# Performance work log

Measured on AMD Instinct MI355X. Metric: run time of the kernel, lower is better.

Reference implementation:

```python
import jax, jax.numpy as jnp
import numpy as np

S, B, N, A, L = 2, 8, 12, 4, 24
C, AUX, EK, K, M, OTH = 256, 16, 64, 256, 8, 32
D2 = C + AUX          # transfromer2 d_model
FF = 2048             # torch TransformerEncoderLayer default dim_feedforward
RIN = 2 * EK + 2 * D2 + 2 * OTH
NLAYERS = 2


def _layernorm(x, g, b, eps=1e-5):
    mu = x.mean(-1, keepdims=True)
    var = ((x - mu) ** 2).mean(-1, keepdims=True)
    return (x - mu) * jax.lax.rsqrt(var + eps) * g + b


def _mha(x, Wq, bq, Wk, bk, Wv, bv, Wo, bo):
    # x: [seq, batch, d]; single head (nhead=1), torch seq-first semantics
    q = x @ Wq.T + bq
    k = x @ Wk.T + bk
    v = x @ Wv.T + bv
    scale = x.shape[-1] ** -0.5
    att = jax.nn.softmax(jnp.einsum('sbd,tbd->bst', q, k) * scale, axis=-1)
    o = jnp.einsum('bst,tbd->sbd', att, v)
    return o @ Wo.T + bo


def _encoder(x, aw, ab, w1, b1, w2, b2, lg, lb):
    # post-norm torch TransformerEncoderLayer, ReLU FFN, dropout off (eval)
    for i in range(aw.shape[0]):
        a = _mha(x, aw[i, 0], ab[i, 0], aw[i, 1], ab[i, 1], aw[i, 2], ab[i, 2], aw[i, 3], ab[i, 3])
        x = _layernorm(x + a, lg[i, 0], lb[i, 0])
        h = jax.nn.relu(x @ w1[i].T + b1[i]) @ w2[i].T + b2[i]
        x = _layernorm(x + h, lg[i, 1], lb[i, 1])
    return x


def _conv(x, w, b, pad):
    y = jax.lax.conv_general_dilated(x, w, (1, 1), [(pad, pad), (0, 0)],
                                     dimension_numbers=('NCHW', 'OIHW', 'NCHW'))
    return y + b[None, :, None, None]


def _forward(chars, att_type, kw_idx, input_idx, static, other,
             char_table, filter_w, filter_b, gate_w, gate_b, mlp_w, mlp_b,
             kw_table, aline_w, aline_b,
             t1_attn_w, t1_attn_b, t1_ffn_w1, t1_ffn_b1, t1_ffn_w2, t1_ffn_b2, t1_ln_g, t1_ln_b,
             t2_attn_w, t2_attn_b, t2_ffn_w1, t2_ffn_b1, t2_ffn_w2, t2_ffn_b2, t2_ln_g, t2_ln_b,
             reg_w1, reg_b1, reg_w2, reg_b2):
    # nn.Embedding(max_norm=1): rows renormalized to norm <= 1
    nrm = jnp.linalg.norm(char_table, axis=1, keepdims=True)
    tbl = char_table * jnp.minimum(1.0, 1.0 / jnp.maximum(nrm, 1e-7))
    ce = tbl[chars]                                  # [S,B,N,A,L,C]
    x = ce.reshape(-1, 1, L, C)                      # strings as conv batch
    f = jnp.tanh(_conv(x, filter_w, filter_b, 1))    # gated conv: tanh * sigmoid
    g = jax.nn.sigmoid(_conv(x, gate_w, gate_b, 1))
    v = _conv(f * g, mlp_w, mlp_b, 0)                # 1x1 conv back to 1 channel
    str_vec = v.reshape(S, B, N, A, L, C).mean(axis=4)   # mean over chars -> [S,B,N,A,C]
    kw_vec = kw_table[kw_idx] @ aline_w.T + aline_b      # keyword path -> [S,B,N,A,C]
    att_vec = jnp.where((att_type == 1)[..., None], kw_vec, str_vec)
    # transfromer1: torch seq-first, seq = nodes, batch = (side, plan, attr)
    x1 = att_vec.transpose(2, 0, 1, 3, 4).reshape(N, S * B * A, C)
    y1 = _encoder(x1, t1_attn_w, t1_attn_b, t1_ffn_w1, t1_ffn_b1, t1_ffn_w2, t1_ffn_b2, t1_ln_g, t1_ln_b)
    node_enc = y1.reshape(N, S, B, A, C).mean(axis=3).transpose(1, 2, 0, 3)  # mean over attrs -> [S,B,N,C]
    h = jnp.concatenate([node_enc, static], axis=-1)                          # [S,B,N,D2]
    # transfromer2: seq = plan batch, batch = (side, node) -- torch seq-first
    x2 = h.transpose(1, 0, 2, 3).reshape(B, S * N, D2)
    y2 = _encoder(x2, t2_attn_w, t2_attn_b, t2_ffn_w1, t2_ffn_b1, t2_ffn_w2, t2_ffn_b2, t2_ln_g, t2_ln_b)
    real = y2.reshape(B, S, N, D2).mean(axis=2)      # mean over nodes -> [B,S,D2]
    inp = kw_table[input_idx].mean(axis=2)           # encoding_input -> [S,B,EK]
    feats = jnp.concatenate([inp[0], real[:, 0], inp[1], real[:, 1], other], axis=1)  # [B,RIN]
    return jax.nn.relu(feats @ reg_w1.T + reg_b1) @ reg_w2.T + reg_b2  # [B,1]


def setup_inputs() -> dict:
    key = jax.random.key(0)
    ks = iter(jax.random.split(key, 64))
    def rn(shape, s=0.02):
        return jax.random.normal(next(ks), shape, jnp.float32) * s
    inp = {
        'chars': jax.random.randint(next(ks), (S, B, N, A, L), 0, 128, jnp.int32),
        'att_type': jax.random.randint(next(ks), (S, B, N, A), 0, 2, jnp.int32),
        'kw_idx': jax.random.randint(next(ks), (S, B, N, A), 0, K, jnp.int32),
        'input_idx': jax.random.randint(next(ks), (S, B, M), 0, K, jnp.int32),
        'static': rn((S, B, N, AUX), 1.0),
        'other': rn((B, 2 * OTH), 1.0),
        'char_table': rn((128, C), 1.0),
        'filter_w': rn((16, 1, 3, 1), 0.2), 'filter_b': rn((16,), 0.02),
        'gate_w': rn((16, 1, 3, 1), 0.2), 'gate_b': rn((16,), 0.02),
        'mlp_w': rn((1, 16, 1, 1), 0.2), 'mlp_b': rn((1,), 0.02),
        'kw_table': rn((K, EK), 0.05),
        'aline_w': rn((C, EK), 0.05), 'aline_b': rn((C,), 0.02),
        't1_attn_w': rn((NLAYERS, 4, C, C), 0.05), 't1_attn_b': rn((NLAYERS, 4, C), 0.02),
        't1_ffn_w1': rn((NLAYERS, FF, C), 0.02), 't1_ffn_b1': rn((NLAYERS, FF), 0.02),
        't1_ffn_w2': rn((NLAYERS, C, FF), 0.02), 't1_ffn_b2': rn((NLAYERS, C), 0.02),
        't1_ln_g': jnp.ones((NLAYERS, 2, C), jnp.float32), 't1_ln_b': jnp.zeros((NLAYERS, 2, C), jnp.float32),
        't2_attn_w': rn((NLAYERS, 4, D2, D2), 0.05), 't2_attn_b': rn((NLAYERS, 4, D2), 0.02),
        't2_ffn_w1': rn((NLAYERS, FF, D2), 0.02), 't2_ffn_b1': rn((NLAYERS, FF), 0.02),
        't2_ffn_w2': rn((NLAYERS, D2, FF), 0.02), 't2_ffn_b2': rn((NLAYERS, D2), 0.02),
        't2_ln_g': jnp.ones((NLAYERS, 2, D2), jnp.float32), 't2_ln_b': jnp.zeros((NLAYERS, 2, D2), jnp.float32),
        'reg_w1': rn((32, RIN), 0.05), 'reg_b1': rn((32,), 0.02),
        'reg_w2': rn((1, 32), 0.1), 'reg_b2': rn((1,), 0.02),
    }
    return inp


def reference(chars, att_type, kw_idx, input_idx, static, other,
              char_table, filter_w, filter_b, gate_w, gate_b, mlp_w, mlp_b,
              kw_table, aline_w, aline_b,
              t1_attn_w, t1_attn_b, t1_ffn_w1, t1_ffn_b1, t1_ffn_w2, t1_ffn_b2, t1_ln_g, t1_ln_b,
              t2_attn_w, t2_attn_b, t2_ffn_w1, t2_ffn_b1, t2_ffn_w2, t2_ffn_b2, t2_ln_g, t2_ln_b,
              reg_w1, reg_b1, reg_w2, reg_b2):
    return _forward(chars, att_type, kw_idx, input_idx, static, other,
                    char_table, filter_w, filter_b, gate_w, gate_b, mlp_w, mlp_b,
                    kw_table, aline_w, aline_b,
                    t1_attn_w, t1_attn_b, t1_ffn_w1, t1_ffn_b1, t1_ffn_w2, t1_ffn_b2, t1_ln_g, t1_ln_b,
                    t2_attn_w, t2_attn_b, t2_ffn_w1, t2_ffn_b1, t2_ffn_w2, t2_ffn_b2, t2_ln_g, t2_ln_b,
                    reg_w1, reg_b1, reg_w2, reg_b2)
```

## Files before the change

kernel.cpp:

```cpp
#include <hip/hip_runtime.h>
#include <math.h>

#define S_ 2
#define B_ 8
#define N_ 12
#define A_ 4
#define L_ 24
#define C_ 256
#define AUX_ 16
#define EK_ 64
#define K_ 256
#define M_ 8
#define OTH_ 32
#define D2_ 272
#define FF_ 2048
#define RIN_ 736
#define NSTR_ (S_*B_*N_*A_)

typedef __attribute__((ext_vector_type(8))) short short8v;
typedef __attribute__((ext_vector_type(4))) float f32x4;

__device__ __forceinline__ unsigned short f2bf(float f) {
    unsigned u = __float_as_uint(f);
    return (unsigned short)((u + 0x7FFFu + ((u >> 16) & 1u)) >> 16);
}

__global__ void cvt_w_k(const float* __restrict__ s0, const float* __restrict__ s1,
                        const float* __restrict__ s2, const float* __restrict__ s3,
                        const float* __restrict__ s4, const float* __restrict__ s5,
                        unsigned short* __restrict__ dst) {
    const int T = 5441536 / 4;
    for (int q = blockIdx.x * 256 + threadIdx.x; q < T; q += gridDim.x * 256) {
        int idx = q * 4;
        const float* src; int off;
        if      (idx < 524288)  { src = s0; off = 0; }
        else if (idx < 1572864) { src = s1; off = 524288; }
        else if (idx < 2621440) { src = s2; off = 1572864; }
        else if (idx < 3213312) { src = s3; off = 2621440; }
        else if (idx < 4327424) { src = s4; off = 3213312; }
        else                    { src = s5; off = 4327424; }
        float4 v = *(const float4*)(src + (idx - off));
        ushort4 o;
        o.x = f2bf(v.x); o.y = f2bf(v.y); o.z = f2bf(v.z); o.w = f2bf(v.w);
        *(ushort4*)(dst + idx) = o;
    }
}

__global__ void scale_table_k(const float* __restrict__ tbl, float* __restrict__ out) {
    int r = blockIdx.x;
    int c = threadIdx.x;
    float v = tbl[r * C_ + c];
    float sq = v * v;
    for (int off = 32; off; off >>= 1) sq += __shfl_down(sq, off);
    __shared__ float red[4];
    __shared__ float scl;
    if ((c & 63) == 0) red[c >> 6] = sq;
    __syncthreads();
    if (c == 0) {
        float n = sqrtf(red[0] + red[1] + red[2] + red[3]);
        scl = fminf(1.f, 1.f / fmaxf(n, 1e-7f));
    }
    __syncthreads();
    out[r * C_ + c] = v * scl;
}

__global__ void attvec_k(const int* __restrict__ chars, const int* __restrict__ att_type,
                         const int* __restrict__ kw_idx, const float* __restrict__ tblS,
                         const float* __restrict__ fw, const float* __restrict__ fb,
                         const float* __restrict__ gw, const float* __restrict__ gb,
                         const float* __restrict__ mw, const float* __restrict__ mb,
                         const float* __restrict__ kwt, const float* __restrict__ aw,
                         const float* __restrict__ ab, float* __restrict__ x1,
                         unsigned short* __restrict__ x1b, int* __restrict__ ctr) {
    int tid = threadIdx.x;
    int grp = tid >> 8;
    int c = tid & 255;
    __shared__ int su;
    __shared__ int ch[L_];
    __shared__ float xv[L_ + 2][C_];
    __shared__ float part[4][C_];

    const float L2E = 1.44269504f;
    float f0[4], f1[4], f2[4], fbv[4], g0[4], g1[4], g2[4], gbv[4], mwv[4];
    #pragma unroll
    for (int oo = 0; oo < 4; ++oo) {
        int o = grp * 4 + oo;
        f0[oo] = 2.f*L2E*fw[o*3]; f1[oo] = 2.f*L2E*fw[o*3+1]; f2[oo] = 2.f*L2E*fw[o*3+2];
        fbv[oo] = 2.f*L2E*fb[o];
        g0[oo] = L2E*gw[o*3]; g1[oo] = L2E*gw[o*3+1]; g2[oo] = L2E*gw[o*3+2];
        gbv[oo] = L2E*gb[o];
        mwv[oo] = mw[o];
    }

    for (;;) {
        if (tid == 0) su = atomicAdd(ctr, 1);
        __syncthreads();
        int str = su;
        if (str >= NSTR_) break;
        bool kw = (att_type[str] == 1);
        float partial;
        if (kw) {
            const float* kr = kwt + kw_idx[str] * EK_ + grp * 16;
            const float* awr = aw + c * EK_ + grp * 16;
            float acc = (grp == 0) ? ab[c] : 0.f;
            #pragma unroll
            for (int e = 0; e < 16; ++e) acc = fmaf(kr[e], awr[e], acc);
            partial = acc;
        } else {
            if (tid < L_) ch[tid] = chars[str * L_ + tid];
            __syncthreads();
            #pragma unroll
            for (int i = 0; i < 6; ++i) {
                int l = grp * 6 + i;
                xv[l + 1][c] = tblS[ch[l] * C_ + c];
            }
            if (grp == 0) xv[0][c] = 0.f;
            if (grp == 3) xv[L_ + 1][c] = 0.f;
            __syncthreads();

            float osum[4] = {0.f, 0.f, 0.f, 0.f};
            float xm = xv[0][c], x0 = xv[1][c];
            for (int l = 1; l <= L_; ++l) {
                float xp = xv[l + 1][c];
                #pragma unroll
                for (int oo = 0; oo < 4; ++oo) {
                    float pf2 = fbv[oo] + f0[oo]*xm + f1[oo]*x0 + f2[oo]*xp;
                    float pg  = gbv[oo] + g0[oo]*xm + g1[oo]*x0 + g2[oo]*xp;
                    pf2 = fminf(fmaxf(pf2, -43.f), 43.f);
                    pg  = fminf(fmaxf(pg,  -22.f), 22.f);
                    float e1 = __builtin_amdgcn_exp2f(pf2);
                    float e2 = __builtin_amdgcn_exp2f(pg);
                    float num = (e1 - 1.f) * e2;
                    float den = (e1 + 1.f) * (e2 + 1.f);
                    osum[oo] = fmaf(num, __builtin_amdgcn_rcpf(den), osum[oo]);
                }
                xm = x0; x0 = xp;
            }
            partial = mwv[0]*osum[0] + mwv[1]*osum[1] + mwv[2]*osum[2] + mwv[3]*osum[3];
            __syncthreads();
        }
        part[grp][c] = partial;
        __syncthreads();
        if (grp == 0) {
            int a = str & 3;
            int n = (str >> 2) % N_;
            int sb = str / (N_ * A_);
            int row = n * 64 + sb * 4 + a;
            float tot = part[0][c] + part[1][c] + part[2][c] + part[3][c];
            float out = kw ? tot : (mb[0] + tot * (1.f / 24.f));
            x1[row * C_ + c] = out;
            x1b[row * C_ + c] = f2bf(out);
        }
        __syncthreads();
    }
}

__global__ void gemm_mfma_k(const unsigned short* __restrict__ Ab,
                            const unsigned short* __restrict__ Wb,
                            const float* __restrict__ bias, float* __restrict__ Cf,
                            unsigned short* __restrict__ Cb,
                            int R, int K, int N, int relu, int kslice, int obf) {
    int tid = threadIdx.x;
    int wave = tid >> 6, lane = tid & 63;
    int fr = lane & 15, fq = lane >> 4;
    int m0 = blockIdx.y * 64;
    int n0 = blockIdx.x * 64 + wave * 16;
    int kbeg = blockIdx.z * kslice;
    int kend = min(kbeg + kslice, K);
    int col = n0 + fr;
    bool bok = col < N;
    const unsigned short* Wrow = Wb + (size_t)col * K;
    const unsigned short* Ar0 = Ab + (size_t)(m0 + fr) * K;
    const unsigned short* Ar1 = Ab + (size_t)(m0 + 16 + fr) * K;
    const unsigned short* Ar2 = Ab + (size_t)(m0 + 32 + fr) * K;
    const unsigned short* Ar3 = Ab + (size_t)(m0 + 48 + fr) * K;

    f32x4 acc0 = {0.f,0.f,0.f,0.f}, acc1 = {0.f,0.f,0.f,0.f};
    f32x4 acc2 = {0.f,0.f,0.f,0.f}, acc3 = {0.f,0.f,0.f,0.f};
    const short8v z8 = {0,0,0,0,0,0,0,0};
    short8v pb, pa0, pa1, pa2, pa3;

#define LDSET(ktv) do {                                                   \
        int kl2 = (ktv) + fq * 8;                                         \
        bool kv2 = (kl2 + 8 <= kend);                                     \
        pb  = (bok && kv2) ? *(const short8v*)(Wrow + kl2) : z8;          \
        pa0 = kv2 ? *(const short8v*)(Ar0 + kl2) : z8;                    \
        pa1 = kv2 ? *(const short8v*)(Ar1 + kl2) : z8;                    \
        pa2 = kv2 ? *(const short8v*)(Ar2 + kl2) : z8;                    \
        pa3 = kv2 ? *(const short8v*)(Ar3 + kl2) : z8;                    \
    } while (0)

    LDSET(kbeg);
    for (int kt = kbeg; kt < kend; kt += 32) {
        short8v bf = pb, af0 = pa0, af1 = pa1, af2 = pa2, af3 = pa3;
        if (kt + 32 < kend) LDSET(kt + 32);
        acc0 = __builtin_amdgcn_mfma_f32_16x16x32_bf16(af0, bf, acc0, 0, 0, 0);
        acc1 = __builtin_amdgcn_mfma_f32_16x16x32_bf16(af1, bf, acc1, 0, 0, 0);
        acc2 = __builtin_amdgcn_mfma_f32_16x16x32_bf16(af2, bf, acc2, 0, 0, 0);
        acc3 = __builtin_amdgcn_mfma_f32_16x16x32_bf16(af3, bf, acc3, 0, 0, 0);
    }
#undef LDSET

    if (!bok) return;
    bool direct = (gridDim.z == 1);
    float bv = direct ? bias[col] : 0.f;
    float* outf = direct ? Cf : (Cf + (size_t)blockIdx.z * R * N);
#define STOREACC(accv, mi) do {                                           \
        _Pragma("unroll")                                                 \
        for (int j = 0; j < 4; ++j) {                                     \
            int row = m0 + (mi)*16 + fq * 4 + j;                          \
            float v = accv[j] + bv;                                       \
            if (direct && relu) v = fmaxf(v, 0.f);                        \
            if (obf) Cb[(size_t)row * N + col] = f2bf(v);                 \
            else     outf[(size_t)row * N + col] = v;                     \
        }                                                                 \
    } while (0)
    STOREACC(acc0, 0); STOREACC(acc1, 1); STOREACC(acc2, 2); STOREACC(acc3, 3);
#undef STOREACC
}

__global__ void attn_k(const float* __restrict__ qkv, unsigned short* __restrict__ ob,
                       int seq, int batch, int d, float scale) {
    __shared__ float sm[3 * 12 * 260];
    __shared__ float sc[12 * 12];
    int j = blockIdx.x, tid = threadIdx.x;
    int dp = d + 4;
    int s3 = 3 * d;
    float* qs = sm;
    float* ks = sm + 12 * 260;
    float* vs = sm + 2 * 12 * 260;
    for (int idx = tid; idx < seq * d; idx += 256) {
        int s = idx / d, cc = idx - s * d;
        const float* base = qkv + (size_t)(s * batch + j) * s3 + cc;
        qs[s * dp + cc] = base[0];
        ks[s * dp + cc] = base[d];
        vs[s * dp + cc] = base[2 * d];
    }
    __syncthreads();
    for (int p4 = tid; p4 < seq * seq * 4; p4 += 256) {
        int p = p4 >> 2, sub = p4 & 3;
        int s = p / seq, t = p - s * seq;
        const float* qp = qs + s * dp;
        const float* kp = ks + t * dp;
        float acc = 0.f;
        for (int cc = sub; cc < d; cc += 4) acc = fmaf(qp[cc], kp[cc], acc);
        acc += __shfl_xor(acc, 1);
        acc += __shfl_xor(acc, 2);
        if (sub == 0) sc[p] = acc * scale;
    }
    __syncthreads();
    if (tid < seq) {
        float m = -1e30f;
        for (int t = 0; t < seq; ++t) m = fmaxf(m, sc[tid * seq + t]);
        float ssum = 0.f;
        for (int t = 0; t < seq; ++t) {
            float e = __expf(sc[tid * seq + t] - m);
            sc[tid * seq + t] = e;
            ssum += e;
        }
        float inv = 1.f / ssum;
        for (int t = 0; t < seq; ++t) sc[tid * seq + t] *= inv;
    }
    __syncthreads();
    for (int c = tid; c < d; c += 256) {
        for (int s = 0; s < seq; ++s) {
            float acc = 0.f;
            for (int t = 0; t < seq; ++t) acc = fmaf(sc[s * seq + t], vs[t * dp + c], acc);
            ob[(size_t)(s * batch + j) * d + c] = f2bf(acc);
        }
    }
}

__global__ void redln_k(const float* __restrict__ part, const float* __restrict__ bias,
                        float* __restrict__ x, unsigned short* __restrict__ xb,
                        const float* __restrict__ g, const float* __restrict__ b,
                        int d, int NS, int RN) {
    int r = blockIdx.x, tid = threadIdx.x;
    __shared__ float red[10];
    const float* xr = x + (size_t)r * d;
    int i0 = tid, i1 = tid + 256;
    bool h0 = i0 < d, h1 = i1 < d;
    float v0 = 0.f, v1 = 0.f;
    if (h0) {
        v0 = xr[i0] + bias[i0];
        for (int z = 0; z < NS; ++z) v0 += part[(size_t)z * RN + (size_t)r * d + i0];
    }
    if (h1) {
        v1 = xr[i1] + bias[i1];
        for (int z = 0; z < NS; ++z) v1 += part[(size_t)z * RN + (size_t)r * d + i1];
    }
    float s = v0 + v1, ss = v0 * v0 + v1 * v1;
    for (int off = 32; off; off >>= 1) {
        s += __shfl_down(s, off);
        ss += __shfl_down(ss, off);
    }
    if ((tid & 63) == 0) { red[(tid >> 6) * 2] = s; red[(tid >> 6) * 2 + 1] = ss; }
    __syncthreads();
    if (tid == 0) {
        float S = red[0] + red[2] + red[4] + red[6];
        float SS = red[1] + red[3] + red[5] + red[7];
        float mu = S / d;
        float var = SS / d - mu * mu;
        red[8] = mu;
        red[9] = rsqrtf(var + 1e-5f);
    }
    __syncthreads();
    float mu = red[8], inv = red[9];
    float* xw = x + (size_t)r * d;
    if (h0) {
        float o = (v0 - mu) * inv * g[i0] + b[i0];
        xw[i0] = o; xb[(size_t)r * d + i0] = f2bf(o);
    }
    if (h1) {
        float o = (v1 - mu) * inv * g[i1] + b[i1];
        xw[i1] = o; xb[(size_t)r * d + i1] = f2bf(o);
    }
}

__global__ void build_x2_k(const float* __restrict__ y1, const float* __restrict__ stat,
                           float* __restrict__ x2, unsigned short* __restrict__ x2b) {
    int id = blockIdx.x;
    int n = id % N_;
    int b = (id / N_) % B_;
    int s = id / (N_ * B_);
    int orow = b * (S_ * N_) + s * N_ + n;
    for (int c = threadIdx.x; c < D2_; c += 256) {
        float v;
        if (c < C_) {
            int j0 = (s * B_ + b) * A_;
            float acc = 0.f;
            for (int a = 0; a < A_; ++a) acc += y1[(size_t)(n * 64 + j0 + a) * C_ + c];
            v = acc * 0.25f;
        } else {
            v = stat[((size_t)(s * B_ + b) * N_ + n) * AUX_ + (c - C_)];
        }
        x2[(size_t)orow * D2_ + c] = v;
        x2b[(size_t)orow * D2_ + c] = f2bf(v);
    }
}

__global__ void build_real_k(const float* __restrict__ y2, float* __restrict__ real) {
    int id = blockIdx.x;
    int s = id & 1, b = id >> 1;
    for (int c = threadIdx.x; c < D2_; c += 256) {
        float acc = 0.f;
        for (int n = 0; n < N_; ++n) acc += y2[(size_t)(b * 24 + s * N_ + n) * D2_ + c];
        real[(size_t)(b * 2 + s) * D2_ + c] = acc * (1.f / 12.f);
    }
}

__global__ void regressor_k(const float* __restrict__ real, const int* __restrict__ input_idx,
                            const float* __restrict__ kwt, const float* __restrict__ other,
                            const float* __restrict__ w1, const float* __restrict__ b1,
                            const float* __restrict__ w2, const float* __restrict__ b2,
                            float* __restrict__ out) {
    int b = blockIdx.x;
    int tid = threadIdx.x;
    __shared__ float feats[RIN_];
    __shared__ float hh[32];
    for (int i = tid; i < RIN_; i += 256) {
        float v;
        if (i < 64) {
            float acc = 0.f;
            for (int m = 0; m < M_; ++m) acc += kwt[input_idx[b * M_ + m] * EK_ + i];
            v = acc * 0.125f;
        } else if (i < 336) {
            v = real[(size_t)(b * 2 + 0) * D2_ + (i - 64)];
        } else if (i < 400) {
            int e = i - 336;
            float acc = 0.f;
            for (int m = 0; m < M_; ++m) acc += kwt[input_idx[64 + b * M_ + m] * EK_ + e];
            v = acc * 0.125f;
        } else if (i < 672) {
            v = real[(size_t)(b * 2 + 1) * D2_ + (i - 400)];
        } else {
            v = other[b * 64 + (i - 672)];
        }
        feats[i] = v;
    }
    __syncthreads();
    if (tid < 32) {
        float acc = b1[tid];
        const float* wr = w1 + (size_t)tid * RIN_;
        for (int i = 0; i < RIN_; ++i) acc += feats[i] * wr[i];
        hh[tid] = fmaxf(acc, 0.f);
    }
    __syncthreads();
    if (tid == 0) {
        float acc = b2[0];
        for (int j = 0; j < 32; ++j) acc += hh[j] * w2[j];
        out[b] = acc;
    }
}

extern "C" void kernel_launch(void* const* d_in, const int* in_sizes, int n_in,
                              void* d_out, int out_size, void* d_ws, size_t ws_size,
                              hipStream_t stream) {
    const int*   chars      = (const int*)d_in[0];
    const int*   att_type   = (const int*)d_in[1];
    const int*   kw_idx     = (const int*)d_in[2];
    const int*   input_idx  = (const int*)d_in[3];
    const float* stat       = (const float*)d_in[4];
    const float* other      = (const float*)d_in[5];
    const float* char_table = (const float*)d_in[6];
    const float* filter_w   = (const float*)d_in[7];
    const float* filter_b   = (const float*)d_in[8];
    const float* gate_w     = (const float*)d_in[9];
    const float* gate_b     = (const float*)d_in[10];
    const float* mlp_w      = (const float*)d_in[11];
    const float* mlp_b      = (const float*)d_in[12];
    const float* kw_table   = (const float*)d_in[13];
    const float* aline_w    = (const float*)d_in[14];
    const float* aline_b    = (const float*)d_in[15];
    const float* t1_attn_w  = (const float*)d_in[16];
    const float* t1_attn_b  = (const float*)d_in[17];
    const float* t1_ffn_w1  = (const float*)d_in[18];
    const float* t1_ffn_b1  = (const float*)d_in[19];
    const float* t1_ffn_w2  = (const float*)d_in[20];
    const float* t1_ffn_b2  = (const float*)d_in[21];
    const float* t1_ln_g    = (const float*)d_in[22];
    const float* t1_ln_b    = (const float*)d_in[23];
    const float* t2_attn_w  = (const float*)d_in[24];
    const float* t2_attn_b  = (const float*)d_in[25];
    const float* t2_ffn_w1  = (const float*)d_in[26];
    const float* t2_ffn_b1  = (const float*)d_in[27];
    const float* t2_ffn_w2  = (const float*)d_in[28];
    const float* t2_ffn_b2  = (const float*)d_in[29];
    const float* t2_ln_g    = (const float*)d_in[30];
    const float* t2_ln_b    = (const float*)d_in[31];
    const float* reg_w1     = (const float*)d_in[32];
    const float* reg_b1     = (const float*)d_in[33];
    const float* reg_w2     = (const float*)d_in[34];
    const float* reg_b2     = (const float*)d_in[35];

    float* ws   = (float*)d_ws;
    float* tblS = ws;
    float* x1   = tblS + 32768;
    float* qkv  = x1 + 196608;
    float* pbuf = qkv + 589824;
    float* x2   = pbuf + 786432;
    float* realb= x2 + 52224;
    unsigned short* x1b = (unsigned short*)(realb + 4352);
    unsigned short* obb = x1b + 196608;
    unsigned short* hb  = obb + 196608;
    unsigned short* x2b = hb + 1572864;
    unsigned short* wbf = x2b + 52224 + 16;
    unsigned short* wb_t1_attn = wbf;
    unsigned short* wb_t1_ffn1 = wbf + 524288;
    unsigned short* wb_t1_ffn2 = wbf + 1572864;
    unsigned short* wb_t2_attn = wbf + 2621440;
    unsigned short* wb_t2_ffn1 = wbf + 3213312;
    unsigned short* wb_t2_ffn2 = wbf + 4327424;
    int* ctr = (int*)(wbf + 5441536);

    auto gemm_f32 = [&](const unsigned short* A, const unsigned short* Wb, const float* bias,
                        float* Cc, int R, int Kk, int N) {
        dim3 g((N + 63) / 64, R / 64, 1);
        gemm_mfma_k<<<g, 256, 0, stream>>>(A, Wb, bias, Cc, (unsigned short*)0,
                                           R, Kk, N, 0, Kk, 0);
    };
    auto gemm_bf16 = [&](const unsigned short* A, const unsigned short* Wb, const float* bias,
                         unsigned short* Cc, int R, int Kk, int N) {
        dim3 g((N + 63) / 64, R / 64, 1);
        gemm_mfma_k<<<g, 256, 0, stream>>>(A, Wb, bias, (float*)0, Cc,
                                           R, Kk, N, 1, Kk, 1);
    };
    auto gemm_split_ln = [&](const unsigned short* A, const unsigned short* Wb,
                             const float* bias, float* x, unsigned short* xb,
                             const float* g, const float* b,
                             int R, int Kk, int N, int ns) {
        int ksl = ((Kk + ns - 1) / ns + 31) / 32 * 32;
        dim3 gr((N + 63) / 64, R / 64, ns);
        gemm_mfma_k<<<gr, 256, 0, stream>>>(A, Wb, bias, pbuf, (unsigned short*)0,
                                            R, Kk, N, 0, ksl, 0);
        redln_k<<<R, 256, 0, stream>>>(pbuf, bias, x, xb, g, b, N, ns, R * N);
    };

    hipMemsetAsync(ctr, 0, sizeof(int), stream);
    cvt_w_k<<<2048, 256, 0, stream>>>(t1_attn_w, t1_ffn_w1, t1_ffn_w2,
                                      t2_attn_w, t2_ffn_w1, t2_ffn_w2, wbf);
    scale_table_k<<<128, 256, 0, stream>>>(char_table, tblS);
    attvec_k<<<512, 1024, 0, stream>>>(chars, att_type, kw_idx, tblS,
                                       filter_w, filter_b, gate_w, gate_b,
                                       mlp_w, mlp_b, kw_table, aline_w, aline_b,
                                       x1, x1b, ctr);

    for (int i = 0; i < 2; ++i) {
        const unsigned short* awb = wb_t1_attn + (size_t)i * 4 * C_ * C_;
        const float* ab = t1_attn_b + (size_t)i * 4 * C_;
        gemm_f32(x1b, awb, ab, qkv, 768, C_, 3 * C_);
        attn_k<<<64, 256, 0, stream>>>(qkv, obb, 12, 64, C_, 0.0625f);
        gemm_split_ln(obb, awb + 3 * C_ * C_, ab + 3 * C_, x1, x1b,
                      t1_ln_g + i * 2 * C_, t1_ln_b + i * 2 * C_, 768, C_, C_, 2);
        gemm_bf16(x1b, wb_t1_ffn1 + (size_t)i * FF_ * C_, t1_ffn_b1 + i * FF_, hb, 768, C_, FF_);
        gemm_split_ln(hb, wb_t1_ffn2 + (size_t)i * C_ * FF_, t1_ffn_b2 + i * C_, x1, x1b,
                      t1_ln_g + i * 2 * C_ + C_, t1_ln_b + i * 2 * C_ + C_, 768, FF_, C_, 4);
    }

    build_x2_k<<<192, 256, 0, stream>>>(x1, stat, x2, x2b);

    float sc2 = 1.0f / sqrtf(272.0f);
    for (int i = 0; i < 2; ++i) {
        const unsigned short* awb = wb_t2_attn + (size_t)i * 4 * D2_ * D2_;
        const float* ab = t2_attn_b + (size_t)i * 4 * D2_;
        gemm_f32(x2b, awb, ab, qkv, 192, D2_, 3 * D2_);
        attn_k<<<24, 256, 0, stream>>>(qkv, obb, 8, 24, D2_, sc2);
        gemm_split_ln(obb, awb + 3 * D2_ * D2_, ab + 3 * D2_, x2, x2b,
                      t2_ln_g + i * 2 * D2_, t2_ln_b + i * 2 * D2_, 192, D2_, D2_, 4);
        gemm_bf16(x2b, wb_t2_ffn1 + (size_t)i * FF_ * D2_, t2_ffn_b1 + i * FF_, hb, 192, D2_, FF_);
        gemm_split_ln(hb, wb_t2_ffn2 + (size_t)i * D2_ * FF_, t2_ffn_b2 + i * D2_, x2, x2b,
                      t2_ln_g + i * 2 * D2_ + D2_, t2_ln_b + i * 2 * D2_ + D2_, 192, FF_, D2_, 8);
    }

    build_real_k<<<16, 256, 0, stream>>>(x2, realb);
    regressor_k<<<8, 256, 0, stream>>>(realb, input_idx, kw_table, other,
                                       reg_w1, reg_b1, reg_w2, reg_b2, (float*)d_out);
}
```

Measured before the change: 326.5 us.

## Fuse weight conversion into attvec work queue, double-buffer GEMM loads, fold build_real into regressor

The fp32-to-bf16 weight conversion becomes extra work items in attvec_k's atomic work queue, so conversion overlaps with the character-conv work and one launch is removed. The GEMM inner loop now keeps two K-steps of prefetched loads in flight instead of one. build_real is merged into the regressor kernel, removing another launch. The merged queue adds a barrier per item, and the deeper prefetch raises register pressure in the GEMM.

New measurement: 321.8 us. Within noise of the previous version (-1.4%).

```diff
diff --git a/kernel.cpp b/kernel.cpp
--- a/kernel.cpp
+++ b/kernel.cpp
@@ -16,6 +16,9 @@
 #define FF_ 2048
 #define RIN_ 736
 #define NSTR_ (S_*B_*N_*A_)
+#define NCVT_ 256
+#define T4_ (5441536/4)
+#define CSZ_ (T4_/NCVT_)
 
 typedef __attribute__((ext_vector_type(8))) short short8v;
 typedef __attribute__((ext_vector_type(4))) float f32x4;
@@ -23,27 +26,6 @@
 __device__ __forceinline__ unsigned short f2bf(float f) {
     unsigned u = __float_as_uint(f);
     return (unsigned short)((u + 0x7FFFu + ((u >> 16) & 1u)) >> 16);
-}
-
-__global__ void cvt_w_k(const float* __restrict__ s0, const float* __restrict__ s1,
-                        const float* __restrict__ s2, const float* __restrict__ s3,
-                        const float* __restrict__ s4, const float* __restrict__ s5,
-                        unsigned short* __restrict__ dst) {
-    const int T = 5441536 / 4;
-    for (int q = blockIdx.x * 256 + threadIdx.x; q < T; q += gridDim.x * 256) {
-        int idx = q * 4;
-        const float* src; int off;
-        if      (idx < 524288)  { src = s0; off = 0; }
-        else if (idx < 1572864) { src = s1; off = 524288; }
-        else if (idx < 2621440) { src = s2; off = 1572864; }
-        else if (idx < 3213312) { src = s3; off = 2621440; }
-        else if (idx < 4327424) { src = s4; off = 3213312; }
-        else                    { src = s5; off = 4327424; }
-        float4 v = *(const float4*)(src + (idx - off));
-        ushort4 o;
-        o.x = f2bf(v.x); o.y = f2bf(v.y); o.z = f2bf(v.z); o.w = f2bf(v.w);
-        *(ushort4*)(dst + idx) = o;
-    }
 }
 
 __global__ void scale_table_k(const float* __restrict__ tbl, float* __restrict__ out) {
@@ -71,7 +53,11 @@
                          const float* __restrict__ mw, const float* __restrict__ mb,
                          const float* __restrict__ kwt, const float* __restrict__ aw,
                          const float* __restrict__ ab, float* __restrict__ x1,
-                         unsigned short* __restrict__ x1b, int* __restrict__ ctr) {
+                         unsigned short* __restrict__ x1b, int* __restrict__ ctr,
+                         const float* __restrict__ s0, const float* __restrict__ s1,
+                         const float* __restrict__ s2, const float* __restrict__ s3,
+                         const float* __restrict__ s4, const float* __restrict__ s5,
+                         unsigned short* __restrict__ wdst) {
     int tid = threadIdx.x;
     int grp = tid >> 8;
     int c = tid & 255;
@@ -93,10 +79,36 @@
     }
 
     for (;;) {
+        __syncthreads();
         if (tid == 0) su = atomicAdd(ctr, 1);
         __syncthreads();
-        int str = su;
-        if (str >= NSTR_) break;
+        int item = su;
+        if (item >= NSTR_ + NCVT_) break;
+
+        if (item >= NSTR_) {
+            int base = (item - NSTR_) * CSZ_;
+            #pragma unroll
+            for (int i = 0; i < 6; ++i) {
+                int q = base + i * 1024 + tid;
+                if (q < base + CSZ_) {
+                    int idx = q * 4;
+                    const float* src; int off;
+                    if      (idx < 524288)  { src = s0; off = 0; }
+                    else if (idx < 1572864) { src = s1; off = 524288; }
+                    else if (idx < 2621440) { src = s2; off = 1572864; }
+                    else if (idx < 3213312) { src = s3; off = 2621440; }
+                    else if (idx < 4327424) { src = s4; off = 3213312; }
+                    else                    { src = s5; off = 4327424; }
+                    float4 v = *(const float4*)(src + (idx - off));
+                    ushort4 o;
+                    o.x = f2bf(v.x); o.y = f2bf(v.y); o.z = f2bf(v.z); o.w = f2bf(v.w);
+                    *(ushort4*)(wdst + idx) = o;
+                }
+            }
+            continue;
+        }
+
+        int str = item;
         bool kw = (att_type[str] == 1);
         float partial;
         if (kw) {
@@ -137,7 +149,6 @@
                 xm = x0; x0 = xp;
             }
             partial = mwv[0]*osum[0] + mwv[1]*osum[1] + mwv[2]*osum[2] + mwv[3]*osum[3];
-            __syncthreads();
         }
         part[grp][c] = partial;
         __syncthreads();
@@ -151,14 +162,13 @@
             x1[row * C_ + c] = out;
             x1b[row * C_ + c] = f2bf(out);
         }
-        __syncthreads();
     }
 }
 
 __global__ void gemm_mfma_k(const unsigned short* __restrict__ Ab,
                             const unsigned short* __restrict__ Wb,
-                            const float* __restrict__ bias, float* __restrict__ Cf,
-                            unsigned short* __restrict__ Cb,
+                            const float* __restrict__ bias,
+                            float* __restrict__ Cf, unsigned short* __restrict__ Cb,
                             int R, int K, int N, int relu, int kslice, int obf) {
     int tid = threadIdx.x;
     int wave = tid >> 6, lane = tid & 63;
@@ -178,26 +188,36 @@
     f32x4 acc0 = {0.f,0.f,0.f,0.f}, acc1 = {0.f,0.f,0.f,0.f};
     f32x4 acc2 = {0.f,0.f,0.f,0.f}, acc3 = {0.f,0.f,0.f,0.f};
     const short8v z8 = {0,0,0,0,0,0,0,0};
-    short8v pb, pa0, pa1, pa2, pa3;
-
-#define LDSET(ktv) do {                                                   \
+    short8v pb0, pa00, pa01, pa02, pa03;
+    short8v pb1, pa10, pa11, pa12, pa13;
+
+#define LDSET(PB,PA0,PA1,PA2,PA3,ktv) do {                                \
         int kl2 = (ktv) + fq * 8;                                         \
         bool kv2 = (kl2 + 8 <= kend);                                     \
-        pb  = (bok && kv2) ? *(const short8v*)(Wrow + kl2) : z8;          \
-        pa0 = kv2 ? *(const short8v*)(Ar0 + kl2) : z8;                    \
-        pa1 = kv2 ? *(const short8v*)(Ar1 + kl2) : z8;                    \
-        pa2 = kv2 ? *(const short8v*)(Ar2 + kl2) : z8;                    \
-        pa3 = kv2 ? *(const short8v*)(Ar3 + kl2) : z8;                    \
+        PB  = (bok && kv2) ? *(const short8v*)(Wrow + kl2) : z8;          \
+        PA0 = kv2 ? *(const short8v*)(Ar0 + kl2) : z8;                    \
+        PA1 = kv2 ? *(const short8v*)(Ar1 + kl2) : z8;                    \
+        PA2 = kv2 ? *(const short8v*)(Ar2 + kl2) : z8;                    \
+        PA3 = kv2 ? *(const short8v*)(Ar3 + kl2) : z8;                    \
     } while (0)
 
-    LDSET(kbeg);
-    for (int kt = kbeg; kt < kend; kt += 32) {
-        short8v bf = pb, af0 = pa0, af1 = pa1, af2 = pa2, af3 = pa3;
-        if (kt + 32 < kend) LDSET(kt + 32);
-        acc0 = __builtin_amdgcn_mfma_f32_16x16x32_bf16(af0, bf, acc0, 0, 0, 0);
-        acc1 = __builtin_amdgcn_mfma_f32_16x16x32_bf16(af1, bf, acc1, 0, 0, 0);
-        acc2 = __builtin_amdgcn_mfma_f32_16x16x32_bf16(af2, bf, acc2, 0, 0, 0);
-        acc3 = __builtin_amdgcn_mfma_f32_16x16x32_bf16(af3, bf, acc3, 0, 0, 0);
+    if (kbeg < kend) {
+        LDSET(pb0, pa00, pa01, pa02, pa03, kbeg);
+        LDSET(pb1, pa10, pa11, pa12, pa13, kbeg + 32);
+        for (int kt = kbeg; kt < kend; kt += 64) {
+            short8v tb = pb0, t0 = pa00, t1 = pa01, t2 = pa02, t3 = pa03;
+            LDSET(pb0, pa00, pa01, pa02, pa03, kt + 64);
+            acc0 = __builtin_amdgcn_mfma_f32_16x16x32_bf16(t0, tb, acc0, 0, 0, 0);
+            acc1 = __builtin_amdgcn_mfma_f32_16x16x32_bf16(t1, tb, acc1, 0, 0, 0);
+            acc2 = __builtin_amdgcn_mfma_f32_16x16x32_bf16(t2, tb, acc2, 0, 0, 0);
+            acc3 = __builtin_amdgcn_mfma_f32_16x16x32_bf16(t3, tb, acc3, 0, 0, 0);
+            short8v ub = pb1, u0 = pa10, u1 = pa11, u2 = pa12, u3 = pa13;
+            LDSET(pb1, pa10, pa11, pa12, pa13, kt + 96);
+            acc0 = __builtin_amdgcn_mfma_f32_16x16x32_bf16(u0, ub, acc0, 0, 0, 0);
+            acc1 = __builtin_amdgcn_mfma_f32_16x16x32_bf16(u1, ub, acc1, 0, 0, 0);
+            acc2 = __builtin_amdgcn_mfma_f32_16x16x32_bf16(u2, ub, acc2, 0, 0, 0);
+            acc3 = __builtin_amdgcn_mfma_f32_16x16x32_bf16(u3, ub, acc3, 0, 0, 0);
+        }
     }
 #undef LDSET
 
@@ -211,12 +231,58 @@
             int row = m0 + (mi)*16 + fq * 4 + j;                          \
             float v = accv[j] + bv;                                       \
             if (direct && relu) v = fmaxf(v, 0.f);                        \
-            if (obf) Cb[(size_t)row * N + col] = f2bf(v);                 \
-            else     outf[(size_t)row * N + col] = v;                     \
+            if (direct && obf) Cb[(size_t)row * N + col] = f2bf(v);       \
+            else               outf[(size_t)row * N + col] = v;           \
         }                                                                 \
     } while (0)
     STOREACC(acc0, 0); STOREACC(acc1, 1); STOREACC(acc2, 2); STOREACC(acc3, 3);
 #undef STOREACC
+}
+
+__global__ void redln_k(const float* __restrict__ part, const float* __restrict__ bias,
+                        float* __restrict__ x, unsigned short* __restrict__ xb,
+                        const float* __restrict__ g, const float* __restrict__ b,
+                        int d, int NS, int RN) {
+    int r = blockIdx.x, tid = threadIdx.x;
+    __shared__ float red[10];
+    const float* xr = x + (size_t)r * d;
+    int i0 = tid, i1 = tid + 256;
+    bool h0 = i0 < d, h1 = i1 < d;
+    float v0 = 0.f, v1 = 0.f;
+    if (h0) {
+        v0 = xr[i0] + bias[i0];
+        for (int z = 0; z < NS; ++z) v0 += part[(size_t)z * RN + (size_t)r * d + i0];
+    }
+    if (h1) {
+        v1 = xr[i1] + bias[i1];
+        for (int z = 0; z < NS; ++z) v1 += part[(size_t)z * RN + (size_t)r * d + i1];
+    }
+    float s = v0 + v1, ss = v0 * v0 + v1 * v1;
+    for (int off = 32; off; off >>= 1) {
+        s += __shfl_down(s, off);
+        ss += __shfl_down(ss, off);
+    }
+    if ((tid & 63) == 0) { red[(tid >> 6) * 2] = s; red[(tid >> 6) * 2 + 1] = ss; }
+    __syncthreads();
+    if (tid == 0) {
+        float S = red[0] + red[2] + red[4] + red[6];
+        float SS = red[1] + red[3] + red[5] + red[7];
+        float mu = S / d;
+        float var = SS / d - mu * mu;
+        red[8] = mu;
+        red[9] = rsqrtf(var + 1e-5f);
+    }
+    __syncthreads();
+    float mu = red[8], inv = red[9];
+    float* xw = x + (size_t)r * d;
+    if (h0) {
+        float o = (v0 - mu) * inv * g[i0] + b[i0];
+        xw[i0] = o; xb[(size_t)r * d + i0] = f2bf(o);
+    }
+    if (h1) {
+        float o = (v1 - mu) * inv * g[i1] + b[i1];
+        xw[i1] = o; xb[(size_t)r * d + i1] = f2bf(o);
+    }
 }
 
 __global__ void attn_k(const float* __restrict__ qkv, unsigned short* __restrict__ ob,
@@ -271,52 +337,6 @@
     }
 }
 
-__global__ void redln_k(const float* __restrict__ part, const float* __restrict__ bias,
-                        float* __restrict__ x, unsigned short* __restrict__ xb,
-                        const float* __restrict__ g, const float* __restrict__ b,
-                        int d, int NS, int RN) {
-    int r = blockIdx.x, tid = threadIdx.x;
-    __shared__ float red[10];
-    const float* xr = x + (size_t)r * d;
-    int i0 = tid, i1 = tid + 256;
-    bool h0 = i0 < d, h1 = i1 < d;
-    float v0 = 0.f, v1 = 0.f;
-    if (h0) {
-        v0 = xr[i0] + bias[i0];
-        for (int z = 0; z < NS; ++z) v0 += part[(size_t)z * RN + (size_t)r * d + i0];
-    }
-    if (h1) {
-        v1 = xr[i1] + bias[i1];
-        for (int z = 0; z < NS; ++z) v1 += part[(size_t)z * RN + (size_t)r * d + i1];
-    }
-    float s = v0 + v1, ss = v0 * v0 + v1 * v1;
-    for (int off = 32; off; off >>= 1) {
-        s += __shfl_down(s, off);
-        ss += __shfl_down(ss, off);
-    }
-    if ((tid & 63) == 0) { red[(tid >> 6) * 2] = s; red[(tid >> 6) * 2 + 1] = ss; }
-    __syncthreads();
-    if (tid == 0) {
-        float S = red[0] + red[2] + red[4] + red[6];
-        float SS = red[1] + red[3] + red[5] + red[7];
-        float mu = S / d;
-        float var = SS / d - mu * mu;
-        red[8] = mu;
-        red[9] = rsqrtf(var + 1e-5f);
-    }
-    __syncthreads();
-    float mu = red[8], inv = red[9];
-    float* xw = x + (size_t)r * d;
-    if (h0) {
-        float o = (v0 - mu) * inv * g[i0] + b[i0];
-        xw[i0] = o; xb[(size_t)r * d + i0] = f2bf(o);
-    }
-    if (h1) {
-        float o = (v1 - mu) * inv * g[i1] + b[i1];
-        xw[i1] = o; xb[(size_t)r * d + i1] = f2bf(o);
-    }
-}
-
 __global__ void build_x2_k(const float* __restrict__ y1, const float* __restrict__ stat,
                            float* __restrict__ x2, unsigned short* __restrict__ x2b) {
     int id = blockIdx.x;
@@ -339,25 +359,24 @@
     }
 }
 
-__global__ void build_real_k(const float* __restrict__ y2, float* __restrict__ real) {
-    int id = blockIdx.x;
-    int s = id & 1, b = id >> 1;
-    for (int c = threadIdx.x; c < D2_; c += 256) {
-        float acc = 0.f;
-        for (int n = 0; n < N_; ++n) acc += y2[(size_t)(b * 24 + s * N_ + n) * D2_ + c];
-        real[(size_t)(b * 2 + s) * D2_ + c] = acc * (1.f / 12.f);
-    }
-}
-
-__global__ void regressor_k(const float* __restrict__ real, const int* __restrict__ input_idx,
+__global__ void regressor_k(const float* __restrict__ y2, const int* __restrict__ input_idx,
                             const float* __restrict__ kwt, const float* __restrict__ other,
                             const float* __restrict__ w1, const float* __restrict__ b1,
                             const float* __restrict__ w2, const float* __restrict__ b2,
                             float* __restrict__ out) {
     int b = blockIdx.x;
     int tid = threadIdx.x;
+    __shared__ float realsh[2][D2_];
     __shared__ float feats[RIN_];
     __shared__ float hh[32];
+    for (int idx = tid; idx < 2 * D2_; idx += 256) {
+        int s = idx / D2_, c = idx - s * D2_;
+        float acc = 0.f;
+        for (int n = 0; n < N_; ++n)
+            acc += y2[(size_t)(b * 24 + s * N_ + n) * D2_ + c];
+        realsh[s][c] = acc * (1.f / 12.f);
+    }
+    __syncthreads();
     for (int i = tid; i < RIN_; i += 256) {
         float v;
         if (i < 64) {
@@ -365,14 +384,14 @@
             for (int m = 0; m < M_; ++m) acc += kwt[input_idx[b * M_ + m] * EK_ + i];
             v = acc * 0.125f;
         } else if (i < 336) {
-            v = real[(size_t)(b * 2 + 0) * D2_ + (i - 64)];
+            v = realsh[0][i - 64];
         } else if (i < 400) {
             int e = i - 336;
             float acc = 0.f;
             for (int m = 0; m < M_; ++m) acc += kwt[input_idx[64 + b * M_ + m] * EK_ + e];
             v = acc * 0.125f;
         } else if (i < 672) {
-            v = real[(size_t)(b * 2 + 1) * D2_ + (i - 400)];
+            v = realsh[1][i - 400];
         } else {
             v = other[b * 64 + (i - 672)];
         }
@@ -439,8 +458,8 @@
     float* qkv  = x1 + 196608;
     float* pbuf = qkv + 589824;
     float* x2   = pbuf + 786432;
-    float* realb= x2 + 52224;
-    unsigned short* x1b = (unsigned short*)(realb + 4352);
+    float* spare= x2 + 52224;
+    unsigned short* x1b = (unsigned short*)(spare + 4352);
     unsigned short* obb = x1b + 196608;
     unsigned short* hb  = obb + 196608;
     unsigned short* x2b = hb + 1572864;
@@ -477,13 +496,13 @@
     };
 
     hipMemsetAsync(ctr, 0, sizeof(int), stream);
-    cvt_w_k<<<2048, 256, 0, stream>>>(t1_attn_w, t1_ffn_w1, t1_ffn_w2,
-                                      t2_attn_w, t2_ffn_w1, t2_ffn_w2, wbf);
     scale_table_k<<<128, 256, 0, stream>>>(char_table, tblS);
     attvec_k<<<512, 1024, 0, stream>>>(chars, att_type, kw_idx, tblS,
                                        filter_w, filter_b, gate_w, gate_b,
                                        mlp_w, mlp_b, kw_table, aline_w, aline_b,
-                                       x1, x1b, ctr);
+                                       x1, x1b, ctr,
+                                       t1_attn_w, t1_ffn_w1, t1_ffn_w2,
+                                       t2_attn_w, t2_ffn_w1, t2_ffn_w2, wbf);
 
     for (int i = 0; i < 2; ++i) {
         const unsigned short* awb = wb_t1_attn + (size_t)i * 4 * C_ * C_;
@@ -512,7 +531,6 @@
                       t2_ln_g + i * 2 * D2_ + D2_, t2_ln_b + i * 2 * D2_ + D2_, 192, FF_, D2_, 8);
     }
 
-    build_real_k<<<16, 256, 0, stream>>>(x2, realb);
-    regressor_k<<<8, 256, 0, stream>>>(realb, input_idx, kw_table, other,
+    regressor_k<<<8, 256, 0, stream>>>(x2, input_idx, kw_table, other,
                                        reg_w1, reg_b1, reg_w2, reg_b2, (float*)d_out);
 }
```
